# Kernel tuning notes

Hardware: AMD Instinct MI355X
Metric: run time of the kernel (lower is better)

Reference implementation:

```python
import jax, jax.numpy as jnp
import numpy as np

H = 4  # num_heads


def transformer_conv(x, src, dst, wq, bq, wk, bk, wv, bv, ws, bs):
    # PyG TransformerConv, concat=False, root_weight=True, eval mode (no dropout).
    N = x.shape[0]
    C = wq.shape[1] // H  # per-head channels
    q = (x @ wq + bq).reshape(N, H, C)
    k = (x @ wk + bk).reshape(N, H, C)
    v = (x @ wv + bv).reshape(N, H, C)
    # per-edge attention logits: query at dst, key at src
    logits = (q[dst] * k[src]).sum(-1) / jnp.sqrt(jnp.asarray(C, x.dtype))  # [E,H]
    # scatter-softmax over incoming edges of each destination node
    m = jax.lax.stop_gradient(jax.ops.segment_max(logits, dst, num_segments=N))
    m = jnp.where(jnp.isfinite(m), m, jnp.zeros_like(m))
    e = jnp.exp(logits - m[dst])
    denom = jax.ops.segment_sum(e, dst, num_segments=N)
    alpha = e / (denom[dst] + 1e-16)  # [E,H]
    out = jax.ops.segment_sum(alpha[:, :, None] * v[src], dst, num_segments=N)  # [N,H,C]
    return out.mean(axis=1) + x @ ws + bs  # head-average + skip


def setup_inputs() -> dict:
    key = jax.random.key(0)
    ks = jax.random.split(key, 16)
    N, E, D, HID, OUT = 50000, 800000, 128, 32, 40
    s = 0.05
    inp = {
        "x": jax.random.normal(ks[0], (N, D), jnp.float32),
        "edge_index": jax.random.randint(ks[1], (2, E), 0, N, jnp.int64),
        "wq1": jax.random.normal(ks[2], (D, H * HID), jnp.float32) * s,
        "bq1": jnp.zeros((H * HID,), jnp.float32),
        "wk1": jax.random.normal(ks[3], (D, H * HID), jnp.float32) * s,
        "bk1": jnp.zeros((H * HID,), jnp.float32),
        "wv1": jax.random.normal(ks[4], (D, H * HID), jnp.float32) * s,
        "bv1": jnp.zeros((H * HID,), jnp.float32),
        "ws1": jax.random.normal(ks[5], (D, HID), jnp.float32) * s,
        "bs1": jnp.zeros((HID,), jnp.float32),
        "wq2": jax.random.normal(ks[6], (HID, H * HID), jnp.float32) * s,
        "bq2": jnp.zeros((H * HID,), jnp.float32),
        "wk2": jax.random.normal(ks[7], (HID, H * HID), jnp.float32) * s,
        "bk2": jnp.zeros((H * HID,), jnp.float32),
        "wv2": jax.random.normal(ks[8], (HID, H * HID), jnp.float32) * s,
        "bv2": jnp.zeros((H * HID,), jnp.float32),
        "ws2": jax.random.normal(ks[9], (HID, HID), jnp.float32) * s,
        "bs2": jnp.zeros((HID,), jnp.float32),
        "wc": jax.random.normal(ks[10], (HID, OUT), jnp.float32) * s,
        "bc": jnp.zeros((OUT,), jnp.float32),
    }
    return inp


def reference(x, edge_index, wq1, bq1, wk1, bk1, wv1, bv1, ws1, bs1,
              wq2, bq2, wk2, bk2, wv2, bv2, ws2, bs2, wc, bc):
    src, dst = edge_index[0], edge_index[1]
    h = jax.nn.relu(transformer_conv(x, src, dst, wq1, bq1, wk1, bk1, wv1, bv1, ws1, bs1))
    h = jax.nn.relu(transformer_conv(h, src, dst, wq2, bq2, wk2, bk2, wv2, bv2, ws2, bs2))
    return h @ wc + bc
```

## Files before the change

kernel.cpp:

```cpp
#include <hip/hip_runtime.h>
#include <hip/hip_bf16.h>

typedef __attribute__((ext_vector_type(8))) short short8;
typedef __attribute__((ext_vector_type(4))) float floatx4;
typedef __attribute__((ext_vector_type(4))) unsigned short ushort4v;

__device__ inline unsigned short f2bf(float x) {
    unsigned int u = __float_as_uint(x);
    u += 0x7FFFu + ((u >> 16) & 1u);
    return (unsigned short)(u >> 16);
}
__device__ inline float bf2f(unsigned short h) {
    return __uint_as_float(((unsigned int)h) << 16);
}

__global__ __launch_bounds__(256) void hist_kernel(
    const int* __restrict__ dst, int* __restrict__ deg, int E)
{
    int e = blockIdx.x * blockDim.x + threadIdx.x;
    if (e < E) atomicAdd(&deg[dst[e]], 1);
}

__global__ __launch_bounds__(256) void scan_part(
    const int* __restrict__ deg, int* __restrict__ bsum, int N)
{
    __shared__ int ws[4];
    const int base = blockIdx.x * 1024;
    const int tid = threadIdx.x, lane = tid & 63, w = tid >> 6;
    int s = 0;
#pragma unroll
    for (int j = 0; j < 4; j++) {
        int i = base + j * 256 + tid;
        if (i < N) s += deg[i];
    }
#pragma unroll
    for (int off = 1; off < 64; off <<= 1) s += __shfl_xor(s, off, 64);
    if (lane == 0) ws[w] = s;
    __syncthreads();
    if (tid == 0) bsum[blockIdx.x] = ws[0] + ws[1] + ws[2] + ws[3];
}

__global__ __launch_bounds__(64) void scan_tops(
    const int* __restrict__ bsum, int* __restrict__ boff,
    int* __restrict__ rowptr, int nb, int N)
{
    int lane = threadIdx.x;
    int v = (lane < nb) ? bsum[lane] : 0;
    int inc = v;
#pragma unroll
    for (int off = 1; off < 64; off <<= 1) {
        int t = __shfl_up(inc, off, 64);
        if (lane >= off) inc += t;
    }
    if (lane < nb) boff[lane] = inc - v;
    if (lane == 63) rowptr[N] = inc;
}

__global__ __launch_bounds__(256) void scan_final(
    const int* __restrict__ deg, const int* __restrict__ boff,
    int* __restrict__ rowptr, int* __restrict__ cursor, int N)
{
    __shared__ int woff[4];
    const int base = blockIdx.x * 1024;
    const int tid = threadIdx.x, lane = tid & 63, w = tid >> 6;
    const int i0 = base + tid * 4;
    int v0 = (i0     < N) ? deg[i0]     : 0;
    int v1 = (i0 + 1 < N) ? deg[i0 + 1] : 0;
    int v2 = (i0 + 2 < N) ? deg[i0 + 2] : 0;
    int v3 = (i0 + 3 < N) ? deg[i0 + 3] : 0;
    int ts = v0 + v1 + v2 + v3;
    int inc = ts;
#pragma unroll
    for (int off = 1; off < 64; off <<= 1) {
        int t = __shfl_up(inc, off, 64);
        if (lane >= off) inc += t;
    }
    if (lane == 63) woff[w] = inc;
    __syncthreads();
    int wpre = 0;
    if (w > 0) wpre += woff[0];
    if (w > 1) wpre += woff[1];
    if (w > 2) wpre += woff[2];
    int exc = boff[blockIdx.x] + wpre + inc - ts;
    int p0 = exc, p1 = exc + v0, p2 = p1 + v1, p3 = p2 + v2;
    if (i0     < N) { rowptr[i0]     = p0; cursor[i0]     = p0; }
    if (i0 + 1 < N) { rowptr[i0 + 1] = p1; cursor[i0 + 1] = p1; }
    if (i0 + 2 < N) { rowptr[i0 + 2] = p2; cursor[i0 + 2] = p2; }
    if (i0 + 3 < N) { rowptr[i0 + 3] = p3; cursor[i0 + 3] = p3; }
}

__global__ __launch_bounds__(256) void fill_kernel(
    const int* __restrict__ src, const int* __restrict__ dst,
    int* __restrict__ cursor, int* __restrict__ perm, int E)
{
    int e = blockIdx.x * blockDim.x + threadIdx.x;
    if (e >= E) return;
    int pos = atomicAdd(&cursor[dst[e]], 1);
    perm[pos] = src[e];
}

template <int L>
__global__ void wprep_kernel(
    const float* __restrict__ wq, const float* __restrict__ bq,
    const float* __restrict__ wk, const float* __restrict__ bk,
    const float* __restrict__ wv, const float* __restrict__ bv,
    const float* __restrict__ ws, const float* __restrict__ bs,
    unsigned short* __restrict__ wt_hi, unsigned short* __restrict__ wt_lo,
    float* __restrict__ bias)
{
    int c = blockIdx.x;
    int t = threadIdx.x;
    const float* w; const float* b; int cc, ncols;
    if (c < 384) {
        int m = c >> 7; cc = c & 127; ncols = 128;
        w = (m == 0) ? wq : ((m == 1) ? wk : wv);
        b = (m == 0) ? bq : ((m == 1) ? bk : bv);
    } else {
        cc = c - 384; ncols = 32; w = ws; b = bs;
    }
    float val = w[t * ncols + cc];
    unsigned short h = f2bf(val);
    wt_hi[c * L + t] = h;
    wt_lo[c * L + t] = f2bf(val - bf2f(h));
    if (t == 0) bias[c] = b[cc];
}

template <int L>
__global__ __launch_bounds__(256) void proj_mfma(
    const float* __restrict__ xin,
    const unsigned short* __restrict__ wt_hi,
    const unsigned short* __restrict__ wt_lo,
    const float* __restrict__ bias,
    float* __restrict__ q, unsigned short* __restrict__ kvp,
    float* __restrict__ skip, int N)
{
    constexpr int LP = L + 8;
    constexpr int KS = L / 32;
    constexpr int SI = (32 * (L / 4)) / 256;
    __shared__ unsigned short xh[2][32 * LP];
    __shared__ unsigned short xl[2][32 * LP];
    __shared__ float scr[4][32 * 36];
    const int tid = threadIdx.x, lane = tid & 63, w = tid >> 6;
    const int li = lane & 15, quad = lane >> 4;
    const int slot = __builtin_amdgcn_readfirstlane(blockIdx.y * 4 + w);
    const bool hasT = slot < 13;

    int t0 = 24, t1 = 25;
    if (slot < 4)       { t0 = slot * 2; t1 = t0 + 1; }
    else if (slot < 12) { t0 = 4 + slot; t1 = 12 + slot; }

    short8 Ah[2][KS], Al[2][KS];
    float bias_r[2][4];
    if (hasT) {
#pragma unroll
        for (int ti = 0; ti < 2; ti++) {
            int tt = ti ? t1 : t0;
#pragma unroll
            for (int ks = 0; ks < KS; ks++) {
                long off = (long)(tt * 16 + li) * L + ks * 32 + quad * 8;
                Ah[ti][ks] = *(const short8*)(wt_hi + off);
                Al[ti][ks] = *(const short8*)(wt_lo + off);
            }
#pragma unroll
            for (int r = 0; r < 4; r++)
                bias_r[ti][r] = bias[tt * 16 + quad * 4 + r];
        }
    }

    const int nb0 = blockIdx.x * 256;
    float* myscr = scr[w];
    unsigned int* su = (unsigned int*)myscr;

    float4 xv[SI];
    auto issue_loads = [&](int c) {
#pragma unroll
        for (int s = 0; s < SI; s++) {
            int f = s * 256 + tid;
            int row = f / (L / 4), c4 = (f - row * (L / 4)) * 4;
            int n = nb0 + c * 32 + row;
            xv[s] = (n < N) ? *(const float4*)(xin + (long)n * L + c4)
                            : make_float4(0.f, 0.f, 0.f, 0.f);
        }
    };
    auto cvt_store = [&](int buf) {
#pragma unroll
        for (int s = 0; s < SI; s++) {
            int f = s * 256 + tid;
            int row = f / (L / 4), c4 = (f - row * (L / 4)) * 4;
            unsigned short h0 = f2bf(xv[s].x), h1 = f2bf(xv[s].y),
                           h2 = f2bf(xv[s].z), h3 = f2bf(xv[s].w);
            ushort4v hs = {h0, h1, h2, h3};
            ushort4v ls = {f2bf(xv[s].x - bf2f(h0)), f2bf(xv[s].y - bf2f(h1)),
                           f2bf(xv[s].z - bf2f(h2)), f2bf(xv[s].w - bf2f(h3))};
            *(ushort4v*)(xh[buf] + row * LP + c4) = hs;
            *(ushort4v*)(xl[buf] + row * LP + c4) = ls;
        }
    };

    issue_loads(0);
    cvt_store(0);
    __syncthreads();

    for (int c = 0; c < 8; c++) {
        if (c < 7) issue_loads(c + 1);
        const int n0c = nb0 + c * 32;
        if (hasT) {
            const int buf = c & 1;
#pragma unroll
            for (int half = 0; half < 2; half++) {
                short8 Bh[KS], Bl[KS];
#pragma unroll
                for (int ks = 0; ks < KS; ks++) {
                    int off = (half * 16 + li) * LP + ks * 32 + quad * 8;
                    Bh[ks] = *(const short8*)(xh[buf] + off);
                    Bl[ks] = *(const short8*)(xl[buf] + off);
                }
                floatx4 accv[2];
#pragma unroll
                for (int ti = 0; ti < 2; ti++) {
                    floatx4 acc = {0.f, 0.f, 0.f, 0.f};
#pragma unroll
                    for (int ks = 0; ks < KS; ks++) {
                        acc = __builtin_amdgcn_mfma_f32_16x16x32_bf16(Ah[ti][ks], Bh[ks], acc, 0, 0, 0);
                        acc = __builtin_amdgcn_mfma_f32_16x16x32_bf16(Ah[ti][ks], Bl[ks], acc, 0, 0, 0);
                        acc = __builtin_amdgcn_mfma_f32_16x16x32_bf16(Al[ti][ks], Bh[ks], acc, 0, 0, 0);
                    }
#pragma unroll
                    for (int r = 0; r < 4; r++) acc[r] += bias_r[ti][r];
                    accv[ti] = acc;
                }
                const int row = half * 16 + li;
                if (slot < 4 || slot == 12) {
                    *(floatx4*)(myscr + row * 36 + quad * 4)      = accv[0];
                    *(floatx4*)(myscr + row * 36 + 16 + quad * 4) = accv[1];
                } else {
                    unsigned int k01 = (unsigned int)f2bf(accv[0][0]) | ((unsigned int)f2bf(accv[0][1]) << 16);
                    unsigned int k23 = (unsigned int)f2bf(accv[0][2]) | ((unsigned int)f2bf(accv[0][3]) << 16);
                    unsigned int v01 = (unsigned int)f2bf(accv[1][0]) | ((unsigned int)f2bf(accv[1][1]) << 16);
                    unsigned int v23 = (unsigned int)f2bf(accv[1][2]) | ((unsigned int)f2bf(accv[1][3]) << 16);
                    uint4 pk = make_uint4(k01, v01, k23, v23);
                    *(uint4*)(su + row * 20 + quad * 4) = pk;
                }
            }
            if (slot < 4) {
#pragma unroll
                for (int it = 0; it < 4; it++) {
                    int idx = it * 64 + lane;
                    int nl = idx >> 3, seg = idx & 7;
                    int node = n0c + nl;
                    if (node < N) {
                        floatx4 vv = *(floatx4*)(myscr + nl * 36 + seg * 4);
                        *(floatx4*)(q + (long)node * 128 + slot * 32 + seg * 4) = vv;
                    }
                }
            } else if (slot == 12) {
#pragma unroll
                for (int it = 0; it < 4; it++) {
                    int idx = it * 64 + lane;
                    int nl = idx >> 3, seg = idx & 7;
                    int node = n0c + nl;
                    if (node < N) {
                        floatx4 vv = *(floatx4*)(myscr + nl * 36 + seg * 4);
                        *(floatx4*)(skip + (long)node * 32 + seg * 4) = vv;
                    }
                }
            } else {
                const int i = slot - 4;
#pragma unroll
                for (int it = 0; it < 2; it++) {
                    int idx = it * 64 + lane;
                    int nl = idx >> 2, part = idx & 3;
                    int node = n0c + nl;
                    if (node < N) {
                        uint4 vv = *(uint4*)(su + nl * 20 + part * 4);
                        *(uint4*)((unsigned int*)(kvp + (long)node * 256) + i * 16 + part * 4) = vv;
                    }
                }
            }
        }
        __syncthreads();
        if (c < 7) cvt_store((c + 1) & 1);
        __syncthreads();
    }
}

__global__ __launch_bounds__(256) void attn_kernel(
    const float* __restrict__ q, const unsigned short* __restrict__ kvp,
    const int* __restrict__ rowptr, const int* __restrict__ perm,
    const float* __restrict__ skip, float* __restrict__ h, int N)
{
    const int wid = (blockIdx.x * 256 + threadIdx.x) >> 6;
    const int lane = threadIdx.x & 63;
    if (wid >= N) return;
    const int d = __builtin_amdgcn_readfirstlane(wid);
    const float2 q2 = *(const float2*)(q + (long)d * 128 + lane * 2);
    float m = -INFINITY, den = 0.f;
    float ox = 0.f, oy = 0.f;
    const int beg = rowptr[d], end = rowptr[d + 1];
    const float scale = 0.17677669529663687f;
    int idx = beg;
    for (; idx + 3 < end; idx += 4) {
        int s0 = perm[idx], s1 = perm[idx + 1], s2 = perm[idx + 2], s3 = perm[idx + 3];
        uint2 a0 = *(const uint2*)(kvp + (long)s0 * 256 + lane * 4);
        uint2 a1 = *(const uint2*)(kvp + (long)s1 * 256 + lane * 4);
        uint2 a2 = *(const uint2*)(kvp + (long)s2 * 256 + lane * 4);
        uint2 a3 = *(const uint2*)(kvp + (long)s3 * 256 + lane * 4);
        float p0 = q2.x * __uint_as_float(a0.x << 16) + q2.y * __uint_as_float(a0.x & 0xFFFF0000u);
        float p1 = q2.x * __uint_as_float(a1.x << 16) + q2.y * __uint_as_float(a1.x & 0xFFFF0000u);
        float p2 = q2.x * __uint_as_float(a2.x << 16) + q2.y * __uint_as_float(a2.x & 0xFFFF0000u);
        float p3 = q2.x * __uint_as_float(a3.x << 16) + q2.y * __uint_as_float(a3.x & 0xFFFF0000u);
        p0 += __shfl_xor(p0, 1);  p1 += __shfl_xor(p1, 1);  p2 += __shfl_xor(p2, 1);  p3 += __shfl_xor(p3, 1);
        p0 += __shfl_xor(p0, 2);  p1 += __shfl_xor(p1, 2);  p2 += __shfl_xor(p2, 2);  p3 += __shfl_xor(p3, 2);
        p0 += __shfl_xor(p0, 4);  p1 += __shfl_xor(p1, 4);  p2 += __shfl_xor(p2, 4);  p3 += __shfl_xor(p3, 4);
        p0 += __shfl_xor(p0, 8);  p1 += __shfl_xor(p1, 8);  p2 += __shfl_xor(p2, 8);  p3 += __shfl_xor(p3, 8);
        float l0 = p0 * scale, l1 = p1 * scale, l2 = p2 * scale, l3 = p3 * scale;
        float mb = fmaxf(fmaxf(l0, l1), fmaxf(l2, l3));
        float nm = fmaxf(m, mb);
        float sc = __expf(m - nm);
        float w0 = __expf(l0 - nm), w1 = __expf(l1 - nm),
              w2 = __expf(l2 - nm), w3 = __expf(l3 - nm);
        den = den * sc + ((w0 + w1) + (w2 + w3));
        float vx = w0 * __uint_as_float(a0.y << 16) + w1 * __uint_as_float(a1.y << 16)
                 + w2 * __uint_as_float(a2.y << 16) + w3 * __uint_as_float(a3.y << 16);
        float vy = w0 * __uint_as_float(a0.y & 0xFFFF0000u) + w1 * __uint_as_float(a1.y & 0xFFFF0000u)
                 + w2 * __uint_as_float(a2.y & 0xFFFF0000u) + w3 * __uint_as_float(a3.y & 0xFFFF0000u);
        ox = ox * sc + vx;
        oy = oy * sc + vy;
        m = nm;
    }
    for (; idx < end; idx++) {
        int s0 = perm[idx];
        uint2 a0 = *(const uint2*)(kvp + (long)s0 * 256 + lane * 4);
        float p0 = q2.x * __uint_as_float(a0.x << 16) + q2.y * __uint_as_float(a0.x & 0xFFFF0000u);
        p0 += __shfl_xor(p0, 1);
        p0 += __shfl_xor(p0, 2);
        p0 += __shfl_xor(p0, 4);
        p0 += __shfl_xor(p0, 8);
        float l0 = p0 * scale;
        float nm = fmaxf(m, l0);
        float sc = __expf(m - nm);
        float wt = __expf(l0 - nm);
        den = den * sc + wt;
        ox = ox * sc + wt * __uint_as_float(a0.y << 16);
        oy = oy * sc + wt * __uint_as_float(a0.y & 0xFFFF0000u);
        m = nm;
    }
    float inv = 1.f / (den + 1e-16f);
    ox *= inv; oy *= inv;
    ox += __shfl_xor(ox, 16); oy += __shfl_xor(oy, 16);
    ox += __shfl_xor(ox, 32); oy += __shfl_xor(oy, 32);
    if (lane < 16) {
        float2 sk = *(const float2*)(skip + (long)d * 32 + lane * 2);
        float rx = 0.25f * ox + sk.x;
        float ry = 0.25f * oy + sk.y;
        float2 r = make_float2(rx > 0.f ? rx : 0.f, ry > 0.f ? ry : 0.f);
        *(float2*)(h + (long)d * 32 + lane * 2) = r;
    }
}

__global__ __launch_bounds__(256) void classify_kernel(
    const float* __restrict__ h, const float* __restrict__ wc,
    const float* __restrict__ bc, float* __restrict__ out, int N)
{
    int gid = blockIdx.x * blockDim.x + threadIdx.x;
    if (gid >= N * 40) return;
    int n = gid / 40, o = gid - (gid / 40) * 40;
    float acc = bc[o];
    const float* hr = h + (long)n * 32;
#pragma unroll
    for (int l = 0; l < 32; ++l) acc += hr[l] * wc[l * 40 + o];
    out[gid] = acc;
}

extern "C" void kernel_launch(void* const* d_in, const int* in_sizes, int n_in,
                              void* d_out, int out_size, void* d_ws, size_t ws_size,
                              hipStream_t stream)
{
    const float* x   = (const float*)d_in[0];
    const int* ei    = (const int*)d_in[1];
    const float* wq1 = (const float*)d_in[2];  const float* bq1 = (const float*)d_in[3];
    const float* wk1 = (const float*)d_in[4];  const float* bk1 = (const float*)d_in[5];
    const float* wv1 = (const float*)d_in[6];  const float* bv1 = (const float*)d_in[7];
    const float* ws1 = (const float*)d_in[8];  const float* bs1 = (const float*)d_in[9];
    const float* wq2 = (const float*)d_in[10]; const float* bq2 = (const float*)d_in[11];
    const float* wk2 = (const float*)d_in[12]; const float* bk2 = (const float*)d_in[13];
    const float* wv2 = (const float*)d_in[14]; const float* bv2 = (const float*)d_in[15];
    const float* ws2 = (const float*)d_in[16]; const float* bs2 = (const float*)d_in[17];
    const float* wc  = (const float*)d_in[18]; const float* bc  = (const float*)d_in[19];

    const int N = in_sizes[0] / 128;
    const int E = in_sizes[1] / 2;
    const int* src = ei;
    const int* dst = ei + E;

    char* p = (char*)d_ws;
    auto take = [&](size_t bytes) { char* r = p; p += (bytes + 255) & ~(size_t)255; return r; };
    float* q             = (float*)take((size_t)N * 128 * 4);
    unsigned short* kvp  = (unsigned short*)take((size_t)N * 256 * 2);
    float* skip          = (float*)take((size_t)N * 32 * 4);
    float* h1            = (float*)take((size_t)N * 32 * 4);
    float* h2            = (float*)take((size_t)N * 32 * 4);
    unsigned short* wt1h = (unsigned short*)take(416 * 128 * 2);
    unsigned short* wt1l = (unsigned short*)take(416 * 128 * 2);
    unsigned short* wt2h = (unsigned short*)take(416 * 32 * 2);
    unsigned short* wt2l = (unsigned short*)take(416 * 32 * 2);
    float* bias1         = (float*)take(416 * 4);
    float* bias2         = (float*)take(416 * 4);
    int* deg             = (int*)take((size_t)N * 4);
    int* rowptr          = (int*)take((size_t)(N + 1) * 4);
    int* cursor          = (int*)take((size_t)N * 4);
    int* perm            = (int*)take((size_t)E * 4);
    int* bsum            = (int*)take(64 * 4);
    int* boff            = (int*)take(64 * 4);

    const dim3 projGrid((N + 255) / 256, 4);
    const int eGrid    = (E + 255) / 256;
    const int attnGrid = (N + 3) / 4;
    const int nb       = (N + 1023) / 1024;

    wprep_kernel<128><<<416, 128, 0, stream>>>(wq1, bq1, wk1, bk1, wv1, bv1,
                                               ws1, bs1, wt1h, wt1l, bias1);
    wprep_kernel<32><<<416, 32, 0, stream>>>(wq2, bq2, wk2, bk2, wv2, bv2,
                                             ws2, bs2, wt2h, wt2l, bias2);
    hipMemsetAsync(deg, 0, (size_t)N * 4, stream);
    hist_kernel<<<eGrid, 256, 0, stream>>>(dst, deg, E);
    scan_part<<<nb, 256, 0, stream>>>(deg, bsum, N);
    scan_tops<<<1, 64, 0, stream>>>(bsum, boff, rowptr, nb, N);
    scan_final<<<nb, 256, 0, stream>>>(deg, boff, rowptr, cursor, N);
    fill_kernel<<<eGrid, 256, 0, stream>>>(src, dst, cursor, perm, E);

    proj_mfma<128><<<projGrid, 256, 0, stream>>>(x, wt1h, wt1l, bias1, q, kvp, skip, N);
    attn_kernel<<<attnGrid, 256, 0, stream>>>(q, kvp, rowptr, perm, skip, h1, N);

    proj_mfma<32><<<projGrid, 256, 0, stream>>>(h1, wt2h, wt2l, bias2, q, kvp, skip, N);
    attn_kernel<<<attnGrid, 256, 0, stream>>>(q, kvp, rowptr, perm, skip, h2, N);

    classify_kernel<<<(N * 40 + 255) / 256, 256, 0, stream>>>(h2, wc, bc, (float*)d_out, N);
}
```

Measured before the change: 380.3 us.

## Split attention edges across wave halves and merge the two weight-prep kernels

```diff
diff --git a/kernel.cpp b/kernel.cpp
--- a/kernel.cpp
+++ b/kernel.cpp
@@ -13,6 +13,8 @@
 __device__ inline float bf2f(unsigned short h) {
     return __uint_as_float(((unsigned int)h) << 16);
 }
+__device__ inline float blo(unsigned int u) { return __uint_as_float(u << 16); }
+__device__ inline float bhi(unsigned int u) { return __uint_as_float(u & 0xFFFF0000u); }
 
 __global__ __launch_bounds__(256) void hist_kernel(
     const int* __restrict__ dst, int* __restrict__ deg, int E)
@@ -99,29 +101,46 @@
     perm[pos] = src[e];
 }
 
-template <int L>
-__global__ void wprep_kernel(
-    const float* __restrict__ wq, const float* __restrict__ bq,
-    const float* __restrict__ wk, const float* __restrict__ bk,
-    const float* __restrict__ wv, const float* __restrict__ bv,
-    const float* __restrict__ ws, const float* __restrict__ bs,
-    unsigned short* __restrict__ wt_hi, unsigned short* __restrict__ wt_lo,
-    float* __restrict__ bias)
-{
-    int c = blockIdx.x;
-    int t = threadIdx.x;
+__global__ __launch_bounds__(128) void wprep_all(
+    const float* __restrict__ wq1, const float* __restrict__ bq1,
+    const float* __restrict__ wk1, const float* __restrict__ bk1,
+    const float* __restrict__ wv1, const float* __restrict__ bv1,
+    const float* __restrict__ ws1, const float* __restrict__ bs1,
+    const float* __restrict__ wq2, const float* __restrict__ bq2,
+    const float* __restrict__ wk2, const float* __restrict__ bk2,
+    const float* __restrict__ wv2, const float* __restrict__ bv2,
+    const float* __restrict__ ws2, const float* __restrict__ bs2,
+    unsigned short* __restrict__ wt1h, unsigned short* __restrict__ wt1l,
+    float* __restrict__ bias1,
+    unsigned short* __restrict__ wt2h, unsigned short* __restrict__ wt2l,
+    float* __restrict__ bias2)
+{
+    const int layer = (blockIdx.x >= 416) ? 1 : 0;
+    const int c = blockIdx.x - layer * 416;
+    const int t = threadIdx.x;
+    const int L = layer ? 32 : 128;
+    if (t >= L) return;
     const float* w; const float* b; int cc, ncols;
     if (c < 384) {
         int m = c >> 7; cc = c & 127; ncols = 128;
-        w = (m == 0) ? wq : ((m == 1) ? wk : wv);
-        b = (m == 0) ? bq : ((m == 1) ? bk : bv);
+        if (layer == 0) {
+            w = (m == 0) ? wq1 : ((m == 1) ? wk1 : wv1);
+            b = (m == 0) ? bq1 : ((m == 1) ? bk1 : bv1);
+        } else {
+            w = (m == 0) ? wq2 : ((m == 1) ? wk2 : wv2);
+            b = (m == 0) ? bq2 : ((m == 1) ? bk2 : bv2);
+        }
     } else {
-        cc = c - 384; ncols = 32; w = ws; b = bs;
-    }
+        cc = c - 384; ncols = 32;
+        w = layer ? ws2 : ws1; b = layer ? bs2 : bs1;
+    }
+    unsigned short* wh = layer ? wt2h : wt1h;
+    unsigned short* wl = layer ? wt2l : wt1l;
+    float* bias = layer ? bias2 : bias1;
     float val = w[t * ncols + cc];
     unsigned short h = f2bf(val);
-    wt_hi[c * L + t] = h;
-    wt_lo[c * L + t] = f2bf(val - bf2f(h));
+    wh[c * L + t] = h;
+    wl[c * L + t] = f2bf(val - bf2f(h));
     if (t == 0) bias[c] = b[cc];
 }
 
@@ -293,68 +312,78 @@
     const int lane = threadIdx.x & 63;
     if (wid >= N) return;
     const int d = __builtin_amdgcn_readfirstlane(wid);
-    const float2 q2 = *(const float2*)(q + (long)d * 128 + lane * 2);
+    const int eh = lane >> 5;
+    const int sl = lane & 31;
+    const int hh = sl >> 3;
+    const int g  = sl & 7;
+    const int dimoff = hh * 64 + g * 8;
+    const float4 q4 = *(const float4*)(q + (long)d * 128 + hh * 32 + g * 4);
+    const int beg = rowptr[d], end = rowptr[d + 1];
+    const int n = end - beg;
+    const int na = (n + 1) >> 1;
+    const int my_off = beg + (eh ? na : 0);
+    const int my_cnt = eh ? (n - na) : na;
+    const float scale = 0.17677669529663687f;
     float m = -INFINITY, den = 0.f;
-    float ox = 0.f, oy = 0.f;
-    const int beg = rowptr[d], end = rowptr[d + 1];
-    const float scale = 0.17677669529663687f;
-    int idx = beg;
-    for (; idx + 3 < end; idx += 4) {
-        int s0 = perm[idx], s1 = perm[idx + 1], s2 = perm[idx + 2], s3 = perm[idx + 3];
-        uint2 a0 = *(const uint2*)(kvp + (long)s0 * 256 + lane * 4);
-        uint2 a1 = *(const uint2*)(kvp + (long)s1 * 256 + lane * 4);
-        uint2 a2 = *(const uint2*)(kvp + (long)s2 * 256 + lane * 4);
-        uint2 a3 = *(const uint2*)(kvp + (long)s3 * 256 + lane * 4);
-        float p0 = q2.x * __uint_as_float(a0.x << 16) + q2.y * __uint_as_float(a0.x & 0xFFFF0000u);
-        float p1 = q2.x * __uint_as_float(a1.x << 16) + q2.y * __uint_as_float(a1.x & 0xFFFF0000u);
-        float p2 = q2.x * __uint_as_float(a2.x << 16) + q2.y * __uint_as_float(a2.x & 0xFFFF0000u);
-        float p3 = q2.x * __uint_as_float(a3.x << 16) + q2.y * __uint_as_float(a3.x & 0xFFFF0000u);
-        p0 += __shfl_xor(p0, 1);  p1 += __shfl_xor(p1, 1);  p2 += __shfl_xor(p2, 1);  p3 += __shfl_xor(p3, 1);
-        p0 += __shfl_xor(p0, 2);  p1 += __shfl_xor(p1, 2);  p2 += __shfl_xor(p2, 2);  p3 += __shfl_xor(p3, 2);
-        p0 += __shfl_xor(p0, 4);  p1 += __shfl_xor(p1, 4);  p2 += __shfl_xor(p2, 4);  p3 += __shfl_xor(p3, 4);
-        p0 += __shfl_xor(p0, 8);  p1 += __shfl_xor(p1, 8);  p2 += __shfl_xor(p2, 8);  p3 += __shfl_xor(p3, 8);
-        float l0 = p0 * scale, l1 = p1 * scale, l2 = p2 * scale, l3 = p3 * scale;
-        float mb = fmaxf(fmaxf(l0, l1), fmaxf(l2, l3));
-        float nm = fmaxf(m, mb);
-        float sc = __expf(m - nm);
-        float w0 = __expf(l0 - nm), w1 = __expf(l1 - nm),
-              w2 = __expf(l2 - nm), w3 = __expf(l3 - nm);
-        den = den * sc + ((w0 + w1) + (w2 + w3));
-        float vx = w0 * __uint_as_float(a0.y << 16) + w1 * __uint_as_float(a1.y << 16)
-                 + w2 * __uint_as_float(a2.y << 16) + w3 * __uint_as_float(a3.y << 16);
-        float vy = w0 * __uint_as_float(a0.y & 0xFFFF0000u) + w1 * __uint_as_float(a1.y & 0xFFFF0000u)
-                 + w2 * __uint_as_float(a2.y & 0xFFFF0000u) + w3 * __uint_as_float(a3.y & 0xFFFF0000u);
-        ox = ox * sc + vx;
-        oy = oy * sc + vy;
+    float o0 = 0.f, o1 = 0.f, o2 = 0.f, o3 = 0.f;
+    for (int j = 0; j < na; j += 2) {
+        const bool ok0 = j < my_cnt, ok1 = (j + 1) < my_cnt;
+        const int i0 = ok0 ? (my_off + j) : beg;
+        const int i1 = ok1 ? (my_off + j + 1) : beg;
+        const int s0 = perm[i0], s1 = perm[i1];
+        const uint4 a0 = *(const uint4*)(kvp + (long)s0 * 256 + dimoff);
+        const uint4 a1 = *(const uint4*)(kvp + (long)s1 * 256 + dimoff);
+        float p0 = q4.x * blo(a0.x) + q4.y * bhi(a0.x) + q4.z * blo(a0.z) + q4.w * bhi(a0.z);
+        float p1 = q4.x * blo(a1.x) + q4.y * bhi(a1.x) + q4.z * blo(a1.z) + q4.w * bhi(a1.z);
+        p0 += __shfl_xor(p0, 1);  p1 += __shfl_xor(p1, 1);
+        p0 += __shfl_xor(p0, 2);  p1 += __shfl_xor(p1, 2);
+        p0 += __shfl_xor(p0, 4);  p1 += __shfl_xor(p1, 4);
+        const float l0 = ok0 ? p0 * scale : -INFINITY;
+        const float l1 = ok1 ? p1 * scale : -INFINITY;
+        const float nm = fmaxf(fmaxf(m, fmaxf(l0, l1)), -1e30f);
+        const float sc = __expf(m - nm);
+        const float w0 = __expf(l0 - nm);
+        const float w1 = __expf(l1 - nm);
+        den = den * sc + w0 + w1;
+        o0 = o0 * sc + w0 * blo(a0.y) + w1 * blo(a1.y);
+        o1 = o1 * sc + w0 * bhi(a0.y) + w1 * bhi(a1.y);
+        o2 = o2 * sc + w0 * blo(a0.w) + w1 * blo(a1.w);
+        o3 = o3 * sc + w0 * bhi(a0.w) + w1 * bhi(a1.w);
         m = nm;
     }
-    for (; idx < end; idx++) {
-        int s0 = perm[idx];
-        uint2 a0 = *(const uint2*)(kvp + (long)s0 * 256 + lane * 4);
-        float p0 = q2.x * __uint_as_float(a0.x << 16) + q2.y * __uint_as_float(a0.x & 0xFFFF0000u);
-        p0 += __shfl_xor(p0, 1);
-        p0 += __shfl_xor(p0, 2);
-        p0 += __shfl_xor(p0, 4);
-        p0 += __shfl_xor(p0, 8);
-        float l0 = p0 * scale;
-        float nm = fmaxf(m, l0);
-        float sc = __expf(m - nm);
-        float wt = __expf(l0 - nm);
-        den = den * sc + wt;
-        ox = ox * sc + wt * __uint_as_float(a0.y << 16);
-        oy = oy * sc + wt * __uint_as_float(a0.y & 0xFFFF0000u);
-        m = nm;
-    }
-    float inv = 1.f / (den + 1e-16f);
-    ox *= inv; oy *= inv;
-    ox += __shfl_xor(ox, 16); oy += __shfl_xor(oy, 16);
-    ox += __shfl_xor(ox, 32); oy += __shfl_xor(oy, 32);
-    if (lane < 16) {
-        float2 sk = *(const float2*)(skip + (long)d * 32 + lane * 2);
-        float rx = 0.25f * ox + sk.x;
-        float ry = 0.25f * oy + sk.y;
-        float2 r = make_float2(rx > 0.f ? rx : 0.f, ry > 0.f ? ry : 0.f);
-        *(float2*)(h + (long)d * 32 + lane * 2) = r;
+    {
+        const float mo = __shfl_xor(m, 32);
+        const float dn = __shfl_xor(den, 32);
+        const float b0 = __shfl_xor(o0, 32);
+        const float b1 = __shfl_xor(o1, 32);
+        const float b2 = __shfl_xor(o2, 32);
+        const float b3 = __shfl_xor(o3, 32);
+        const float nm = fmaxf(fmaxf(m, mo), -1e30f);
+        const float sa = __expf(m - nm);
+        const float sb = __expf(mo - nm);
+        den = den * sa + dn * sb;
+        o0 = o0 * sa + b0 * sb;
+        o1 = o1 * sa + b1 * sb;
+        o2 = o2 * sa + b2 * sb;
+        o3 = o3 * sa + b3 * sb;
+    }
+    const float inv = 1.f / (den + 1e-16f);
+    o0 *= inv; o1 *= inv; o2 *= inv; o3 *= inv;
+    o0 += __shfl_xor(o0, 8);  o1 += __shfl_xor(o1, 8);
+    o2 += __shfl_xor(o2, 8);  o3 += __shfl_xor(o3, 8);
+    o0 += __shfl_xor(o0, 16); o1 += __shfl_xor(o1, 16);
+    o2 += __shfl_xor(o2, 16); o3 += __shfl_xor(o3, 16);
+    if (lane < 8) {
+        float4 sk = *(const float4*)(skip + (long)d * 32 + g * 4);
+        float r0 = 0.25f * o0 + sk.x;
+        float r1 = 0.25f * o1 + sk.y;
+        float r2 = 0.25f * o2 + sk.z;
+        float r3 = 0.25f * o3 + sk.w;
+        r0 = r0 > 0.f ? r0 : 0.f;
+        r1 = r1 > 0.f ? r1 : 0.f;
+        r2 = r2 > 0.f ? r2 : 0.f;
+        r3 = r3 > 0.f ? r3 : 0.f;
+        *(float4*)(h + (long)d * 32 + g * 4) = make_float4(r0, r1, r2, r3);
     }
 }
 
@@ -418,10 +447,9 @@
     const int attnGrid = (N + 3) / 4;
     const int nb       = (N + 1023) / 1024;
 
-    wprep_kernel<128><<<416, 128, 0, stream>>>(wq1, bq1, wk1, bk1, wv1, bv1,
-                                               ws1, bs1, wt1h, wt1l, bias1);
-    wprep_kernel<32><<<416, 32, 0, stream>>>(wq2, bq2, wk2, bk2, wv2, bv2,
-                                             ws2, bs2, wt2h, wt2l, bias2);
+    wprep_all<<<832, 128, 0, stream>>>(wq1, bq1, wk1, bk1, wv1, bv1, ws1, bs1,
+                                       wq2, bq2, wk2, bk2, wv2, bv2, ws2, bs2,
+                                       wt1h, wt1l, bias1, wt2h, wt2l, bias2);
     hipMemsetAsync(deg, 0, (size_t)N * 4, stream);
     hist_kernel<<<eGrid, 256, 0, stream>>>(dst, deg, E);
     scan_part<<<nb, 256, 0, stream>>>(deg, bsum, N);
```

Result: no change. 379.5 us (-0.2%).
